# Kernel optimization log

Hardware: AMD Instinct MI355X
Metric: run time of the kernel (lower is better)

The kernel has to match this reference:

```python
import jax, jax.numpy as jnp
import numpy as np


def setup_inputs() -> dict:
    key = jax.random.key(0)
    k1, k2 = jax.random.split(key)
    B, C, H, W = 8, 64, 32, 32
    K = 8192
    x = jax.random.normal(k1, (B, C, H, W), dtype=jnp.float32)
    codebook = jax.random.normal(k2, (K, C), dtype=jnp.float32)
    return {"x": x, "codebook": codebook}


def reference(x, codebook):
    """Faithful JAX version of VQVAE.quantize().

    x:        [B, C, H, W] latent (output of pre_quant_conv)
    codebook: [K, C] embedding weight
    Returns (quant_out [B,C,H,W], commitment_loss, codebook_loss, indices [B,H,W]).
    """
    B, C, H, W = x.shape
    # [B, H, W, C] -> [B, N, C]
    xf = jnp.transpose(x, (0, 2, 3, 1)).reshape(B, H * W, C)

    # Squared pairwise distances (argmin of cdist == argmin of squared dist).
    x2 = jnp.sum(xf * xf, axis=-1, keepdims=True)            # [B, N, 1]
    e2 = jnp.sum(codebook * codebook, axis=-1)               # [K]
    xe = jnp.einsum('bnc,kc->bnk', xf, codebook)             # [B, N, K]
    d2 = x2 + e2[None, None, :] - 2.0 * xe                   # [B, N, K]
    idx = jnp.argmin(d2, axis=-1)                            # [B, N]

    quant = codebook[idx.reshape(-1)]                        # [B*N, C]
    xflat = xf.reshape(-1, C)                                # [B*N, C]

    commitment_loss = jnp.mean((jax.lax.stop_gradient(quant) - xflat) ** 2)
    codebook_loss = jnp.mean((quant - jax.lax.stop_gradient(xflat)) ** 2)

    # Straight-through estimator.
    quant_st = xflat + jax.lax.stop_gradient(quant - xflat)
    quant_out = jnp.transpose(quant_st.reshape(B, H, W, C), (0, 3, 1, 2))
    indices = idx.reshape(B, H, W)
    return quant_out, commitment_loss, codebook_loss, indices
```

## Files before the change

kernel.cpp:

```cpp
#include <hip/hip_runtime.h>


#define N_PTS   8192
#define K_CODES 8192
#define C_DIM   64
#define HWSZ    1024
#define QOUT_N  524288
#define SPLITS  32
#define NCH     4

#define WS_PACK  0
#define WS_CBS   2097152
#define WS_E2H   4194304
#define WS_PART  4227072

typedef __attribute__((ext_vector_type(8))) short    short8;
typedef __attribute__((ext_vector_type(8))) _Float16 half8;
typedef __attribute__((ext_vector_type(4))) float    floatx4;

__device__ __forceinline__ half8 as_h8(short8 v) {
    return __builtin_bit_cast(half8, v);
}
__device__ __forceinline__ void split2(float v, unsigned short& h,
                                       unsigned short& m) {
    _Float16 hh = (_Float16)v;
    float r = v - (float)hh;
    _Float16 mm = (_Float16)r;
    h = __builtin_bit_cast(unsigned short, hh);
    m = __builtin_bit_cast(unsigned short, mm);
}
__device__ __forceinline__ void cp16(const void* g, void* l) {
    __builtin_amdgcn_global_load_lds(
        (const __attribute__((address_space(1))) void*)g,
        (__attribute__((address_space(3))) void*)l, 16, 0, 0);
}

__global__ __launch_bounds__(256)
void vq_prep_kernel(const float* __restrict__ cb,
                    unsigned short* __restrict__ cbS,
                    float* __restrict__ e2h)
{
    const int k = blockIdx.x * 256 + threadIdx.x;
    const float* row = cb + k * C_DIM;
    float s = 0.0f;
    #pragma unroll
    for (int g = 0; g < 8; ++g) {
        float4 a = *(const float4*)(row + g * 8);
        float4 b = *(const float4*)(row + g * 8 + 4);
        float vv[8] = {a.x, a.y, a.z, a.w, b.x, b.y, b.z, b.w};
        unsigned short h8[8], m8[8];
        #pragma unroll
        for (int j = 0; j < 8; ++j) {
            s = fmaf(vv[j], vv[j], s);
            split2(vv[j], h8[j], m8[j]);
        }
        *(uint4*)(cbS + ((size_t)(0 * 8 + g) * 8192 + k) * 8) = *(const uint4*)h8;
        *(uint4*)(cbS + ((size_t)(1 * 8 + g) * 8192 + k) * 8) = *(const uint4*)m8;
    }
    e2h[k] = 0.5f * s;
}

#define SEG_SHORTS 512
#define NSEGS      16
#define BUF_SHORTS 8192
#define NBUF       3

__device__ __forceinline__ void computeTile(const half8 af[4][2][2],
                                            const unsigned short* __restrict__ bsrc,
                                            const float* __restrict__ se2row,
                                            int tl, int quad, int col, int code,
                                            float bestv[4][4], int besti[4][4])
{
    half8 bf[2][2];
    #pragma unroll
    for (int p = 0; p < 2; ++p)
        #pragma unroll
        for (int s = 0; s < 2; ++s) {
            int seg = p * 8 + s * 4 + quad;
            bf[p][s] = as_h8(*(const short8*)(bsrc + seg * SEG_SHORTS + (tl * 16 + col) * 8));
        }
    float me2 = -se2row[tl * 16 + col];

    floatx4 acc[4];
    #pragma unroll
    for (int t = 0; t < 4; ++t) acc[t] = (floatx4){me2, me2, me2, me2};

    #pragma unroll
    for (int s = 0; s < 2; ++s) {
        #pragma unroll
        for (int t = 0; t < 4; ++t)
            acc[t] = __builtin_amdgcn_mfma_f32_16x16x32_f16(af[t][0][s], bf[0][s], acc[t], 0, 0, 0);
        #pragma unroll
        for (int t = 0; t < 4; ++t)
            acc[t] = __builtin_amdgcn_mfma_f32_16x16x32_f16(af[t][0][s], bf[1][s], acc[t], 0, 0, 0);
        #pragma unroll
        for (int t = 0; t < 4; ++t)
            acc[t] = __builtin_amdgcn_mfma_f32_16x16x32_f16(af[t][1][s], bf[0][s], acc[t], 0, 0, 0);
    }

    #pragma unroll
    for (int t = 0; t < 4; ++t)
        #pragma unroll
        for (int r = 0; r < 4; ++r) {
            float sc = acc[t][r];
            bool gt = sc > bestv[t][r];
            bestv[t][r] = gt ? sc   : bestv[t][r];
            besti[t][r] = gt ? code : besti[t][r];
        }
}

__global__ __launch_bounds__(512, 1)
void vq_argmin_kernel(const float* __restrict__ x,
                      const unsigned short* __restrict__ cbS,
                      const float* __restrict__ e2h,
                      unsigned long long* __restrict__ packedS)
{
    __shared__ __align__(16) unsigned short sBuf[NBUF][BUF_SHORTS];
    __shared__ __align__(16) float sE2[256];

    const int tid   = threadIdx.x;
    const int lane  = tid & 63;
    const int w     = tid >> 6;
    const int col   = lane & 15;
    const int quad  = lane >> 4;
    const int mb    = blockIdx.x;
    const int split = blockIdx.y;
    const int m0    = mb * 512 + w * 64;
    const int nb0   = split * 256;

    auto stage = [&](int k0, int buf) {
        unsigned short* dst = &sBuf[buf][0];
        #pragma unroll
        for (int i = 0; i < 2; ++i) {
            int f   = tid + i * 512;
            int seg = f >> 6;
            int l   = f & 63;
            cp16(cbS + ((size_t)seg * 8192 + k0 + l) * 8,
                 dst + seg * SEG_SHORTS + l * 8);
        }
    };

    if (tid < 64)
        cp16(e2h + nb0 + tid * 4, &sE2[tid * 4]);
    stage(nb0, 0);
    stage(nb0 + 64, 1);

    const int bimg = mb >> 1;
    const int hwB  = (mb & 1) * 512 + w * 64;
    const float* xb = x + (size_t)bimg * (C_DIM * HWSZ);
    half8 af[4][2][2];
    #pragma unroll
    for (int t = 0; t < 4; ++t) {
        const int hw = hwB + t * 16 + col;
        #pragma unroll
        for (int s = 0; s < 2; ++s) {
            unsigned short h8[8], m8[8];
            #pragma unroll
            for (int j = 0; j < 8; ++j) {
                float v = xb[(size_t)(s * 32 + quad * 8 + j) * HWSZ + hw];
                split2(v, h8[j], m8[j]);
            }
            af[t][0][s] = as_h8(*(const short8*)h8);
            af[t][1][s] = as_h8(*(const short8*)m8);
        }
    }

    float bestv[4][4];
    int   besti[4][4];
    #pragma unroll
    for (int t = 0; t < 4; ++t)
        #pragma unroll
        for (int r = 0; r < 4; ++r) {
            bestv[t][r] = __uint_as_float(0xFF800000u);
            besti[t][r] = 0;
        }

    __syncthreads();

    int cbuf = 0, pbuf = 2;
    #pragma clang loop unroll(disable)
    for (int ch = 0; ch < NCH; ++ch) {
        if (ch < NCH - 2) stage(nb0 + (ch + 2) * 64, pbuf);
        const unsigned short* bsrc = &sBuf[cbuf][0];
        const float* se2row = &sE2[ch * 64];
        #pragma unroll
        for (int tl = 0; tl < 4; ++tl)
            computeTile(af, bsrc, se2row, tl, quad, col,
                        nb0 + ch * 64 + tl * 16 + col, bestv, besti);
        if (ch < NCH - 1) {
            if (ch == NCH - 2) asm volatile("s_waitcnt vmcnt(0)" ::: "memory");
            else               asm volatile("s_waitcnt vmcnt(2)" ::: "memory");
            __builtin_amdgcn_sched_barrier(0);
            __builtin_amdgcn_s_barrier();
            __builtin_amdgcn_sched_barrier(0);
        }
        cbuf = (cbuf == NBUF - 1) ? 0 : cbuf + 1;
        pbuf = (pbuf == NBUF - 1) ? 0 : pbuf + 1;
    }

    unsigned long long own = 0;
    #pragma unroll
    for (int t = 0; t < 4; ++t)
        #pragma unroll
        for (int r = 0; r < 4; ++r) {
            unsigned u = __float_as_uint(-bestv[t][r]);
            u = ((int)u < 0) ? ~u : (u | 0x80000000u);
            unsigned long long p = ((unsigned long long)u << 32) | (unsigned)besti[t][r];
            #pragma unroll
            for (int msk = 1; msk < 16; msk <<= 1) {
                unsigned long long q = __shfl_xor(p, msk, 64);
                p = (q < p) ? q : p;
            }
            own = (col == t * 4 + r) ? p : own;
        }
    const int mpt = m0 + (col >> 2) * 16 + quad * 4 + (col & 3);
    packedS[(size_t)split * N_PTS + mpt] = own;
}

__global__ __launch_bounds__(256)
void vq_gather_kernel(const float* __restrict__ x,
                      const float* __restrict__ cb,
                      const unsigned long long* __restrict__ packedS,
                      float* __restrict__ out,
                      float* __restrict__ part)
{
    __shared__ unsigned long long sred[8][32];
    const int tid = threadIdx.x;
    const int p   = tid & 31;
    const int sg  = tid >> 5;
    const int n0  = blockIdx.x * 32;
    const int n   = n0 + p;

    {
        unsigned long long v = packedS[(size_t)(sg * 4) * N_PTS + n];
        #pragma unroll
        for (int j = 1; j < 4; ++j) {
            unsigned long long q = packedS[(size_t)(sg * 4 + j) * N_PTS + n];
            v = (q < v) ? q : v;
        }
        sred[sg][p] = v;
    }
    __syncthreads();

    unsigned long long v = sred[0][p];
    #pragma unroll
    for (int s = 1; s < 8; ++s) {
        unsigned long long q = sred[s][p];
        v = (q < v) ? q : v;
    }
    const int idx = (int)(v & 0xFFFFFFFFull);
    if (tid < 32) out[QOUT_N + 2 + n0 + tid] = (float)idx;

    const int c0  = sg * 8;
    const int b   = n >> 10;
    const int hw  = n & 1023;
    const float* xb = x   + (size_t)b * (C_DIM * HWSZ) + hw;
    float*       ob = out + (size_t)b * (C_DIM * HWSZ) + hw;

    float s = 0.0f;
    #pragma unroll
    for (int c4 = 0; c4 < 2; ++c4) {
        float4 q = *(const float4*)(cb + (size_t)idx * C_DIM + c0 + c4 * 4);
        float qa[4] = {q.x, q.y, q.z, q.w};
        #pragma unroll
        for (int j = 0; j < 4; ++j) {
            int c = c0 + c4 * 4 + j;
            float xv = xb[c * HWSZ];
            float d  = qa[j] - xv;
            s = fmaf(d, d, s);
            ob[c * HWSZ] = xv + d;
        }
    }

    #pragma unroll
    for (int off = 32; off > 0; off >>= 1) s += __shfl_down(s, off, 64);
    if ((tid & 63) == 0) part[blockIdx.x * 4 + (tid >> 6)] = s;
}

__global__ __launch_bounds__(256)
void vq_final_kernel(const float* __restrict__ part, float* __restrict__ out)
{
    __shared__ float w[4];
    float s = part[threadIdx.x] + part[threadIdx.x + 256]
            + part[threadIdx.x + 512] + part[threadIdx.x + 768];
    #pragma unroll
    for (int off = 32; off > 0; off >>= 1) s += __shfl_down(s, off, 64);
    if ((threadIdx.x & 63) == 0) w[threadIdx.x >> 6] = s;
    __syncthreads();
    if (threadIdx.x == 0) {
        float m = (w[0] + w[1] + w[2] + w[3]) * (1.0f / (float)QOUT_N);
        out[QOUT_N]     = m;
        out[QOUT_N + 1] = m;
    }
}

extern "C" void kernel_launch(void* const* d_in, const int* in_sizes, int n_in,
                              void* d_out, int out_size, void* d_ws, size_t ws_size,
                              hipStream_t stream)
{
    const float* x  = (const float*)d_in[0];
    const float* cb = (const float*)d_in[1];
    float* out = (float*)d_out;
    char*  ws  = (char*)d_ws;
    (void)ws_size;

    unsigned long long* packedS = (unsigned long long*)(ws + WS_PACK);
    unsigned short* cbS = (unsigned short*)(ws + WS_CBS);
    float* e2h = (float*)(ws + WS_E2H);
    float* part = (float*)(ws + WS_PART);

    vq_prep_kernel<<<32, 256, 0, stream>>>(cb, cbS, e2h);
    vq_argmin_kernel<<<dim3(16, SPLITS), 512, 0, stream>>>(x, cbS, e2h, packedS);
    vq_gather_kernel<<<256, 256, 0, stream>>>(x, cb, packedS, out, part);
    vq_final_kernel<<<1, 256, 0, stream>>>(part, out);
}
```

Measured before the change: 108.2 us.

## Drop LDS staging in argmin kernel and read codebook directly with smaller blocks

The argmin kernel no longer stages codebook tiles into shared memory through a triple-buffered global_load_lds pipeline with barriers. Each wave now loads its B fragments and e2 values straight from global memory (L2/L1), and handles 32 points instead of 64. Blocks shrink to 256 threads, the launch bound allows 4 blocks per CU, and the grid grows fourfold. This removes barriers and LDS traffic and raises occupancy, but halves per-wave reuse of the B fragments and relies on cache hits for repeated codebook reads.

```diff
diff --git a/kernel.cpp b/kernel.cpp
--- a/kernel.cpp
+++ b/kernel.cpp
@@ -29,11 +29,6 @@
     h = __builtin_bit_cast(unsigned short, hh);
     m = __builtin_bit_cast(unsigned short, mm);
 }
-__device__ __forceinline__ void cp16(const void* g, void* l) {
-    __builtin_amdgcn_global_load_lds(
-        (const __attribute__((address_space(1))) void*)g,
-        (__attribute__((address_space(3))) void*)l, 16, 0, 0);
-}
 
 __global__ __launch_bounds__(256)
 void vq_prep_kernel(const float* __restrict__ cb,
@@ -60,64 +55,12 @@
     e2h[k] = 0.5f * s;
 }
 
-#define SEG_SHORTS 512
-#define NSEGS      16
-#define BUF_SHORTS 8192
-#define NBUF       3
-
-__device__ __forceinline__ void computeTile(const half8 af[4][2][2],
-                                            const unsigned short* __restrict__ bsrc,
-                                            const float* __restrict__ se2row,
-                                            int tl, int quad, int col, int code,
-                                            float bestv[4][4], int besti[4][4])
-{
-    half8 bf[2][2];
-    #pragma unroll
-    for (int p = 0; p < 2; ++p)
-        #pragma unroll
-        for (int s = 0; s < 2; ++s) {
-            int seg = p * 8 + s * 4 + quad;
-            bf[p][s] = as_h8(*(const short8*)(bsrc + seg * SEG_SHORTS + (tl * 16 + col) * 8));
-        }
-    float me2 = -se2row[tl * 16 + col];
-
-    floatx4 acc[4];
-    #pragma unroll
-    for (int t = 0; t < 4; ++t) acc[t] = (floatx4){me2, me2, me2, me2};
-
-    #pragma unroll
-    for (int s = 0; s < 2; ++s) {
-        #pragma unroll
-        for (int t = 0; t < 4; ++t)
-            acc[t] = __builtin_amdgcn_mfma_f32_16x16x32_f16(af[t][0][s], bf[0][s], acc[t], 0, 0, 0);
-        #pragma unroll
-        for (int t = 0; t < 4; ++t)
-            acc[t] = __builtin_amdgcn_mfma_f32_16x16x32_f16(af[t][0][s], bf[1][s], acc[t], 0, 0, 0);
-        #pragma unroll
-        for (int t = 0; t < 4; ++t)
-            acc[t] = __builtin_amdgcn_mfma_f32_16x16x32_f16(af[t][1][s], bf[0][s], acc[t], 0, 0, 0);
-    }
-
-    #pragma unroll
-    for (int t = 0; t < 4; ++t)
-        #pragma unroll
-        for (int r = 0; r < 4; ++r) {
-            float sc = acc[t][r];
-            bool gt = sc > bestv[t][r];
-            bestv[t][r] = gt ? sc   : bestv[t][r];
-            besti[t][r] = gt ? code : besti[t][r];
-        }
-}
-
-__global__ __launch_bounds__(512, 1)
+__global__ __launch_bounds__(256, 4)
 void vq_argmin_kernel(const float* __restrict__ x,
                       const unsigned short* __restrict__ cbS,
                       const float* __restrict__ e2h,
                       unsigned long long* __restrict__ packedS)
 {
-    __shared__ __align__(16) unsigned short sBuf[NBUF][BUF_SHORTS];
-    __shared__ __align__(16) float sE2[256];
-
     const int tid   = threadIdx.x;
     const int lane  = tid & 63;
     const int w     = tid >> 6;
@@ -125,33 +68,16 @@
     const int quad  = lane >> 4;
     const int mb    = blockIdx.x;
     const int split = blockIdx.y;
-    const int m0    = mb * 512 + w * 64;
+    const int m0    = mb * 128 + w * 32;
     const int nb0   = split * 256;
 
-    auto stage = [&](int k0, int buf) {
-        unsigned short* dst = &sBuf[buf][0];
-        #pragma unroll
-        for (int i = 0; i < 2; ++i) {
-            int f   = tid + i * 512;
-            int seg = f >> 6;
-            int l   = f & 63;
-            cp16(cbS + ((size_t)seg * 8192 + k0 + l) * 8,
-                 dst + seg * SEG_SHORTS + l * 8);
-        }
-    };
-
-    if (tid < 64)
-        cp16(e2h + nb0 + tid * 4, &sE2[tid * 4]);
-    stage(nb0, 0);
-    stage(nb0 + 64, 1);
-
-    const int bimg = mb >> 1;
-    const int hwB  = (mb & 1) * 512 + w * 64;
+    const int bimg = m0 >> 10;
+    const int hw0  = m0 & 1023;
     const float* xb = x + (size_t)bimg * (C_DIM * HWSZ);
-    half8 af[4][2][2];
-    #pragma unroll
-    for (int t = 0; t < 4; ++t) {
-        const int hw = hwB + t * 16 + col;
+    half8 af[2][2][2];
+    #pragma unroll
+    for (int t = 0; t < 2; ++t) {
+        const int hw = hw0 + t * 16 + col;
         #pragma unroll
         for (int s = 0; s < 2; ++s) {
             unsigned short h8[8], m8[8];
@@ -165,42 +91,64 @@
         }
     }
 
-    float bestv[4][4];
-    int   besti[4][4];
-    #pragma unroll
-    for (int t = 0; t < 4; ++t)
+    float bestv[2][4];
+    int   besti[2][4];
+    #pragma unroll
+    for (int t = 0; t < 2; ++t)
         #pragma unroll
         for (int r = 0; r < 4; ++r) {
             bestv[t][r] = __uint_as_float(0xFF800000u);
             besti[t][r] = 0;
         }
 
-    __syncthreads();
-
-    int cbuf = 0, pbuf = 2;
     #pragma clang loop unroll(disable)
     for (int ch = 0; ch < NCH; ++ch) {
-        if (ch < NCH - 2) stage(nb0 + (ch + 2) * 64, pbuf);
-        const unsigned short* bsrc = &sBuf[cbuf][0];
-        const float* se2row = &sE2[ch * 64];
-        #pragma unroll
-        for (int tl = 0; tl < 4; ++tl)
-            computeTile(af, bsrc, se2row, tl, quad, col,
-                        nb0 + ch * 64 + tl * 16 + col, bestv, besti);
-        if (ch < NCH - 1) {
-            if (ch == NCH - 2) asm volatile("s_waitcnt vmcnt(0)" ::: "memory");
-            else               asm volatile("s_waitcnt vmcnt(2)" ::: "memory");
-            __builtin_amdgcn_sched_barrier(0);
-            __builtin_amdgcn_s_barrier();
-            __builtin_amdgcn_sched_barrier(0);
-        }
-        cbuf = (cbuf == NBUF - 1) ? 0 : cbuf + 1;
-        pbuf = (pbuf == NBUF - 1) ? 0 : pbuf + 1;
+        const int k0 = nb0 + ch * 64;
+        #pragma unroll
+        for (int tl = 0; tl < 4; ++tl) {
+            const int code = k0 + tl * 16 + col;
+            half8 bf[2][2];
+            #pragma unroll
+            for (int p = 0; p < 2; ++p)
+                #pragma unroll
+                for (int s = 0; s < 2; ++s) {
+                    int seg = p * 8 + s * 4 + quad;
+                    bf[p][s] = as_h8(*(const short8*)(cbS + ((size_t)seg * 8192 + code) * 8));
+                }
+            float me2 = -e2h[code];
+
+            floatx4 acc[2];
+            #pragma unroll
+            for (int t = 0; t < 2; ++t) acc[t] = (floatx4){me2, me2, me2, me2};
+
+            #pragma unroll
+            for (int s = 0; s < 2; ++s) {
+                #pragma unroll
+                for (int t = 0; t < 2; ++t)
+                    acc[t] = __builtin_amdgcn_mfma_f32_16x16x32_f16(af[t][0][s], bf[0][s], acc[t], 0, 0, 0);
+                #pragma unroll
+                for (int t = 0; t < 2; ++t)
+                    acc[t] = __builtin_amdgcn_mfma_f32_16x16x32_f16(af[t][0][s], bf[1][s], acc[t], 0, 0, 0);
+                #pragma unroll
+                for (int t = 0; t < 2; ++t)
+                    acc[t] = __builtin_amdgcn_mfma_f32_16x16x32_f16(af[t][1][s], bf[0][s], acc[t], 0, 0, 0);
+            }
+
+            #pragma unroll
+            for (int t = 0; t < 2; ++t)
+                #pragma unroll
+                for (int r = 0; r < 4; ++r) {
+                    float sc = acc[t][r];
+                    bool gt = sc > bestv[t][r];
+                    bestv[t][r] = gt ? sc   : bestv[t][r];
+                    besti[t][r] = gt ? code : besti[t][r];
+                }
+        }
     }
 
     unsigned long long own = 0;
     #pragma unroll
-    for (int t = 0; t < 4; ++t)
+    for (int t = 0; t < 2; ++t)
         #pragma unroll
         for (int r = 0; r < 4; ++r) {
             unsigned u = __float_as_uint(-bestv[t][r]);
@@ -213,8 +161,10 @@
             }
             own = (col == t * 4 + r) ? p : own;
         }
-    const int mpt = m0 + (col >> 2) * 16 + quad * 4 + (col & 3);
-    packedS[(size_t)split * N_PTS + mpt] = own;
+    if (col < 8) {
+        const int mpt = m0 + (col >> 2) * 16 + quad * 4 + (col & 3);
+        packedS[(size_t)split * N_PTS + mpt] = own;
+    }
 }
 
 __global__ __launch_bounds__(256)
@@ -310,7 +260,7 @@
     float* part = (float*)(ws + WS_PART);
 
     vq_prep_kernel<<<32, 256, 0, stream>>>(cb, cbS, e2h);
-    vq_argmin_kernel<<<dim3(16, SPLITS), 512, 0, stream>>>(x, cbS, e2h, packedS);
+    vq_argmin_kernel<<<dim3(64, SPLITS), 256, 0, stream>>>(x, cbS, e2h, packedS);
     vq_gather_kernel<<<256, 256, 0, stream>>>(x, cb, packedS, out, part);
     vq_final_kernel<<<1, 256, 0, stream>>>(part, out);
 }
```

After: 98.28 us. 9.2% less time.
